# Optimization experiments

Hardware: AMD Instinct MI355X
Metric: run time of the kernel (lower is better)

Reference implementation:

```python
import jax, jax.numpy as jnp
import numpy as np

N_NODES = 50000
N_EDGES = 800000
IN_F = 128
HID = 128
OUT = 2


def setup_inputs() -> dict:
    key = jax.random.key(0)
    ks = jax.random.split(key, 10)
    x = jax.random.normal(ks[0], (N_NODES, IN_F), dtype=jnp.float32)
    edge_index = jax.random.randint(ks[1], (2, N_EDGES), 0, N_NODES, dtype=jnp.int64)

    def lin(k, fan_in, fan_out):
        s = 1.0 / np.sqrt(fan_in)
        return jax.random.uniform(k, (fan_in, fan_out), jnp.float32, -s, s)

    return {
        "x": x,
        "edge_index": edge_index,
        # SAGEConv1: lin_l applied to mean-aggregated neighbors (with bias),
        # lin_r applied to root features (no bias), PyG convention.
        "W1_l": lin(ks[2], IN_F, HID),
        "W1_r": lin(ks[3], IN_F, HID),
        "b1": jnp.zeros((HID,), jnp.float32),
        "W2_l": lin(ks[4], HID, HID),
        "W2_r": lin(ks[5], HID, HID),
        "b2": jnp.zeros((HID,), jnp.float32),
        "Wfc": lin(ks[6], HID, OUT),
        "bfc": jnp.zeros((OUT,), jnp.float32),
    }


def reference(x, edge_index, W1_l, W1_r, b1, W2_l, W2_r, b2, Wfc, bfc):
    n = x.shape[0]
    src = edge_index[0]  # message source j
    dst = edge_index[1]  # aggregation target i
    # in-degree for mean aggregation (clamp to avoid div-by-zero for isolated nodes)
    deg = jax.ops.segment_sum(jnp.ones_like(dst, dtype=x.dtype), dst, num_segments=n)
    inv_deg = 1.0 / jnp.maximum(deg, 1.0)  # [n]

    def sage_conv(h, Wl, Wr, b):
        # mean over incoming neighbor features, then two linear maps
        agg = jax.ops.segment_sum(h[src], dst, num_segments=n) * inv_deg[:, None]
        return agg @ Wl + h @ Wr + b

    # dropout is identity at inference (training=False)
    h = jax.nn.relu(sage_conv(x, W1_l, W1_r, b1))
    h = jax.nn.relu(sage_conv(h, W2_l, W2_r, b2))
    return h @ Wfc + bfc  # [n, out] logits
```

## Files before the change

kernel.cpp:

```cpp
#include <hip/hip_runtime.h>

#define NN 50000
#define NE 800000
#define BSHIFT 9
#define NB_BUCKET ((NN + 511) >> BSHIFT)
#define BCAP 16384
#define EPB 2048
#define NBLK_E ((NE + EPB - 1) / EPB)

#define CVT_BLKS 6250
#define PREP_BLKS 32
#define SETUP_GRID (CVT_BLKS + PREP_BLKS + 1)

typedef short short8 __attribute__((ext_vector_type(8)));
typedef short short4v __attribute__((ext_vector_type(4)));
typedef float f32x4 __attribute__((ext_vector_type(4)));

__device__ inline unsigned short bf16_rne(float f) {
    unsigned u = __float_as_uint(f);
    unsigned r = (u + 0x7fffu + ((u >> 16) & 1u)) >> 16;
    return (unsigned short)r;
}
__device__ inline float bf16_to_f32(unsigned short h) {
    return __uint_as_float((unsigned)h << 16);
}

__global__ __launch_bounds__(256) void setup_kernel(const float* __restrict__ x,
                                                    unsigned short* __restrict__ xb,
                                                    const float* __restrict__ W0,
                                                    const float* __restrict__ W1,
                                                    const float* __restrict__ W2,
                                                    const float* __restrict__ W3,
                                                    short* __restrict__ wf,
                                                    int* __restrict__ cursor0) {
    int b = blockIdx.x;
    if (b < CVT_BLKS) {
        int i = b * 256 + threadIdx.x;
        float4 v = ((const float4*)x)[i];
        short4v r;
        r[0] = (short)bf16_rne(v.x);
        r[1] = (short)bf16_rne(v.y);
        r[2] = (short)bf16_rne(v.z);
        r[3] = (short)bf16_rne(v.w);
        ((short4v*)xb)[i] = r;
    } else if (b < CVT_BLKS + PREP_BLKS) {
        int t = (b - CVT_BLKS) * 256 + threadIdx.x;
        int mat = t >> 11;
        const float* W = (mat == 0) ? W0 : (mat == 1) ? W1 : (mat == 2) ? W2 : W3;
        short* out = wf + (size_t)mat * 32768;
        int r = t & 2047;
        int nt = r >> 8;
        int kc = (r >> 6) & 3;
        int lane = r & 63;
        int n = nt * 16 + (lane & 15);
        int kbase = kc * 32 + ((lane >> 4) << 3);
        short8 vh, vl;
#pragma unroll
        for (int j = 0; j < 8; ++j) {
            float w = W[(size_t)(kbase + j) * 128 + n];
            unsigned short h = bf16_rne(w);
            unsigned short l = bf16_rne(w - bf16_to_f32(h));
            vh[j] = (short)h;
            vl[j] = (short)l;
        }
        size_t o = ((((size_t)nt * 4 + kc) * 2) * 64 + lane) * 8;
        *(short8*)(out + o) = vh;
        *(short8*)(out + o + 512) = vl;
    } else {
        if (threadIdx.x < NB_BUCKET) cursor0[threadIdx.x] = 0;
    }
}

__global__ __launch_bounds__(256) void binA_kernel(const int* __restrict__ src,
                                                   const int* __restrict__ dst,
                                                   int* __restrict__ cursor0,
                                                   unsigned* __restrict__ packed, int ne) {
    __shared__ int cnt[NB_BUCKET];
    __shared__ int gstart[NB_BUCKET];
    __shared__ int cur[NB_BUCKET];
    int t = threadIdx.x;
    if (t < NB_BUCKET) cnt[t] = 0;
    __syncthreads();
    int base = blockIdx.x * EPB + t * 8;
    int s[8], d[8];
    int m = 0;
    if (base + 8 <= ne) {
        *(int4*)&s[0] = *(const int4*)(src + base);
        *(int4*)&s[4] = *(const int4*)(src + base + 4);
        *(int4*)&d[0] = *(const int4*)(dst + base);
        *(int4*)&d[4] = *(const int4*)(dst + base + 4);
        m = 8;
    } else if (base < ne) {
        m = ne - base;
        for (int i = 0; i < m; ++i) { s[i] = src[base + i]; d[i] = dst[base + i]; }
    }
    for (int i = 0; i < m; ++i) atomicAdd(&cnt[d[i] >> BSHIFT], 1);
    __syncthreads();
    if (t < NB_BUCKET) {
        gstart[t] = t * BCAP + atomicAdd(&cursor0[t], cnt[t]);
        cur[t] = 0;
    }
    __syncthreads();
    for (int i = 0; i < m; ++i) {
        int b = d[i] >> BSHIFT;
        int l = atomicAdd(&cur[b], 1);
        packed[gstart[b] + l] = ((unsigned)(d[i] & 511) << 16) | (unsigned)s[i];
    }
}

__global__ __launch_bounds__(512) void binB_kernel(const unsigned* __restrict__ packed,
                                                   const int* __restrict__ cursor0,
                                                   int* __restrict__ row_ptr,
                                                   float* __restrict__ inv_deg,
                                                   int* __restrict__ col, int n, int ne) {
    __shared__ int sdeg[512];
    __shared__ int scur[512];
    __shared__ int scnt[NB_BUCKET];
    __shared__ int sebeg[NB_BUCKET];
    int b = blockIdx.x, t = threadIdx.x;
    if (t < NB_BUCKET) scnt[t] = cursor0[t];
    sdeg[t] = 0;
    __syncthreads();
    if (t == 0) {
        int run = 0;
        for (int i = 0; i < NB_BUCKET; ++i) { sebeg[i] = run; run += scnt[i]; }
    }
    __syncthreads();
    int ebeg = sebeg[b];
    int cntE = scnt[b];
    const unsigned* pk = packed + (size_t)b * BCAP;
    for (int e = t; e < cntE; e += 512) atomicAdd(&sdeg[pk[e] >> 16], 1);
    __syncthreads();
    int v = sdeg[t];
    for (int d = 1; d < 512; d <<= 1) {
        int u = (t >= d) ? sdeg[t - d] : 0;
        __syncthreads();
        sdeg[t] += u;
        __syncthreads();
    }
    int excl = sdeg[t] - v;
    scur[t] = excl;
    int node = (b << BSHIFT) + t;
    if (node < n) {
        row_ptr[node] = ebeg + excl;
        inv_deg[node] = 1.0f / (float)(v > 0 ? v : 1);
    }
    if (b == 0 && t == 0) row_ptr[n] = ne;
    __syncthreads();
    for (int e = t; e < cntE; e += 512) {
        unsigned w = pk[e];
        int dl = w >> 16;
        int pos = ebeg + atomicAdd(&scur[dl], 1);
        col[pos] = (int)(w & 0xffffu);
    }
}

__global__ __launch_bounds__(256) void agg_kernel(const unsigned short* __restrict__ hb,
                                                  const int* __restrict__ row_ptr,
                                                  const int* __restrict__ col,
                                                  const float* __restrict__ inv_deg,
                                                  unsigned short* __restrict__ outb, int n) {
    int node = blockIdx.x * 4 + (threadIdx.x >> 6);
    if (node >= n) return;
    int lane = threadIdx.x & 63;
    int slot = lane >> 4, sub = lane & 15;
    int beg = row_ptr[node], end = row_ptr[node + 1];
    const unsigned short* base = hb + (sub << 3);
    float acc[8];
#pragma unroll
    for (int j = 0; j < 8; ++j) acc[j] = 0.f;

    int e = beg + slot;
    for (; e + 4 < end; e += 8) {
        int j0 = col[e];
        int j1 = col[e + 4];
        uint4 v0 = *(const uint4*)(base + ((size_t)j0 << 7));
        uint4 v1 = *(const uint4*)(base + ((size_t)j1 << 7));
        unsigned w0[4] = {v0.x, v0.y, v0.z, v0.w};
        unsigned w1[4] = {v1.x, v1.y, v1.z, v1.w};
#pragma unroll
        for (int d = 0; d < 4; ++d) {
            acc[2 * d + 0] += __uint_as_float(w0[d] << 16);
            acc[2 * d + 1] += __uint_as_float(w0[d] & 0xffff0000u);
            acc[2 * d + 0] += __uint_as_float(w1[d] << 16);
            acc[2 * d + 1] += __uint_as_float(w1[d] & 0xffff0000u);
        }
    }
    if (e < end) {
        int j0 = col[e];
        uint4 v0 = *(const uint4*)(base + ((size_t)j0 << 7));
        unsigned w0[4] = {v0.x, v0.y, v0.z, v0.w};
#pragma unroll
        for (int d = 0; d < 4; ++d) {
            acc[2 * d + 0] += __uint_as_float(w0[d] << 16);
            acc[2 * d + 1] += __uint_as_float(w0[d] & 0xffff0000u);
        }
    }
#pragma unroll
    for (int j = 0; j < 8; ++j) {
        acc[j] += __shfl_xor(acc[j], 16, 64);
        acc[j] += __shfl_xor(acc[j], 32, 64);
    }
    if (slot == 0) {
        float s = inv_deg[node];
        short8 o;
#pragma unroll
        for (int j = 0; j < 8; ++j) o[j] = (short)bf16_rne(acc[j] * s);
        *(short8*)(outb + ((size_t)node << 7) + (sub << 3)) = o;
    }
}

__global__ __launch_bounds__(256) void gemm_mfma(const unsigned short* __restrict__ A0b,
                                                 const unsigned short* __restrict__ A1b,
                                                 const short* __restrict__ Wf0,
                                                 const short* __restrict__ Wf1,
                                                 const float* __restrict__ bias,
                                                 unsigned short* __restrict__ outb,
                                                 const float* __restrict__ Wfc,
                                                 const float* __restrict__ bfc,
                                                 float* __restrict__ fcout,
                                                 int n, int relu) {
    int lane = threadIdx.x & 63;
    int wave = threadIdx.x >> 6;
    int quad = lane >> 4, m16 = lane & 15;
    int row_base = blockIdx.x * 64 + wave * 16;
    int arow = row_base + m16;
    if (arow > n - 1) arow = n - 1;

    f32x4 acc[8];
#pragma unroll
    for (int nt = 0; nt < 8; ++nt) acc[nt] = (f32x4){0.f, 0.f, 0.f, 0.f};

    const unsigned short* ap0 = A0b + ((size_t)arow << 7) + (quad << 3);
    const unsigned short* ap1 = A1b + ((size_t)arow << 7) + (quad << 3);
#pragma unroll
    for (int kc = 0; kc < 4; ++kc) {
        short8 a0 = *(const short8*)(ap0 + kc * 32);
        short8 a1 = *(const short8*)(ap1 + kc * 32);
        const short* wp0 = Wf0 + ((size_t)kc * 2 * 64 + lane) * 8;
        const short* wp1 = Wf1 + ((size_t)kc * 2 * 64 + lane) * 8;
#pragma unroll
        for (int nt = 0; nt < 8; ++nt) {
            short8 bh0 = *(const short8*)(wp0 + (size_t)nt * 4096);
            short8 bl0 = *(const short8*)(wp0 + (size_t)nt * 4096 + 512);
            short8 bh1 = *(const short8*)(wp1 + (size_t)nt * 4096);
            short8 bl1 = *(const short8*)(wp1 + (size_t)nt * 4096 + 512);
            acc[nt] = __builtin_amdgcn_mfma_f32_16x16x32_bf16(a0, bh0, acc[nt], 0, 0, 0);
            acc[nt] = __builtin_amdgcn_mfma_f32_16x16x32_bf16(a0, bl0, acc[nt], 0, 0, 0);
            acc[nt] = __builtin_amdgcn_mfma_f32_16x16x32_bf16(a1, bh1, acc[nt], 0, 0, 0);
            acc[nt] = __builtin_amdgcn_mfma_f32_16x16x32_bf16(a1, bl1, acc[nt], 0, 0, 0);
        }
    }

    float bcol[8];
#pragma unroll
    for (int nt = 0; nt < 8; ++nt) bcol[nt] = bias[nt * 16 + m16];

    if (Wfc) {
        float w0[8], w1[8];
#pragma unroll
        for (int nt = 0; nt < 8; ++nt) {
            float2 wv = *(const float2*)(Wfc + 2 * (nt * 16 + m16));
            w0[nt] = wv.x;
            w1[nt] = wv.y;
        }
        float b0 = bfc[0], b1 = bfc[1];
#pragma unroll
        for (int r = 0; r < 4; ++r) {
            float p0 = 0.f, p1 = 0.f;
#pragma unroll
            for (int nt = 0; nt < 8; ++nt) {
                float v = fmaxf(acc[nt][r] + bcol[nt], 0.f);
                p0 += v * w0[nt];
                p1 += v * w1[nt];
            }
#pragma unroll
            for (int off = 1; off < 16; off <<= 1) {
                p0 += __shfl_xor(p0, off, 64);
                p1 += __shfl_xor(p1, off, 64);
            }
            int row = row_base + quad * 4 + r;
            if (m16 == 0 && row < n) {
                float2 o;
                o.x = p0 + b0;
                o.y = p1 + b1;
                *(float2*)(fcout + 2 * (size_t)row) = o;
            }
        }
    } else {
#pragma unroll
        for (int r = 0; r < 4; ++r) {
            int row = row_base + quad * 4 + r;
            if (row >= n) continue;
            unsigned short* opb = outb + ((size_t)row << 7) + m16;
#pragma unroll
            for (int nt = 0; nt < 8; ++nt) {
                float v = acc[nt][r] + bcol[nt];
                if (relu) v = fmaxf(v, 0.f);
                opb[nt * 16] = bf16_rne(v);
            }
        }
    }
}

extern "C" void kernel_launch(void* const* d_in, const int* in_sizes, int n_in,
                              void* d_out, int out_size, void* d_ws, size_t ws_size,
                              hipStream_t stream) {
    const float* x   = (const float*)d_in[0];
    const int* edge  = (const int*)d_in[1];
    const float* W1l = (const float*)d_in[2];
    const float* W1r = (const float*)d_in[3];
    const float* b1  = (const float*)d_in[4];
    const float* W2l = (const float*)d_in[5];
    const float* W2r = (const float*)d_in[6];
    const float* b2  = (const float*)d_in[7];
    const float* Wfc = (const float*)d_in[8];
    const float* bfc = (const float*)d_in[9];
    float* out = (float*)d_out;

    const int n = NN, ne = NE;
    const int* src = edge;
    const int* dst = edge + ne;

    char* ws = (char*)d_ws;
    size_t off = 0;
    auto alloc = [&](size_t bytes) -> char* {
        char* p = ws + off;
        off = (off + bytes + 511) & ~(size_t)511;
        return p;
    };
    int* row_ptr     = (int*)alloc((size_t)(n + 1) * 4);
    float* invdeg    = (float*)alloc((size_t)n * 4);
    int* cursor0     = (int*)alloc((size_t)NB_BUCKET * 4);
    short* wf        = (short*)alloc((size_t)4 * 32768 * 2);
    unsigned* packed = (unsigned*)alloc((size_t)NB_BUCKET * BCAP * 4);
    int* col         = (int*)alloc((size_t)ne * 4);
    unsigned short* aggb = (unsigned short*)alloc((size_t)n * 128 * 2);
    unsigned short* xb   = (unsigned short*)alloc((size_t)n * 128 * 2);
    unsigned short* h1b  = (unsigned short*)alloc((size_t)n * 128 * 2);
    (void)ws_size; (void)in_sizes; (void)n_in; (void)out_size;

    setup_kernel<<<SETUP_GRID, 256, 0, stream>>>(x, xb, W1l, W1r, W2l, W2r, wf, cursor0);
    binA_kernel<<<NBLK_E, 256, 0, stream>>>(src, dst, cursor0, packed, ne);
    binB_kernel<<<NB_BUCKET, 512, 0, stream>>>(packed, cursor0, row_ptr, invdeg, col, n, ne);

    agg_kernel<<<(n + 3) / 4, 256, 0, stream>>>(xb, row_ptr, col, invdeg, aggb, n);
    gemm_mfma<<<(n + 63) / 64, 256, 0, stream>>>(aggb, xb, wf, wf + 32768, b1, h1b,
                                                 (const float*)0, (const float*)0, (float*)0, n, 1);
    agg_kernel<<<(n + 3) / 4, 256, 0, stream>>>(h1b, row_ptr, col, invdeg, aggb, n);
    gemm_mfma<<<(n + 63) / 64, 256, 0, stream>>>(aggb, h1b, wf + 2 * 32768, wf + 3 * 32768, b2,
                                                 (unsigned short*)0, Wfc, bfc, out, n, 1);
}
```

Measured before the change: 227.2 us.

## Fuse neighbor aggregation into MFMA GEMM per layer via LDS staging

Replaces the separate aggregation and GEMM kernels with one kernel per layer. Each wave aggregates 16 nodes into an LDS tile, and the tile then feeds MFMA directly with swapped operands so the output is transposed. This removes the aggregated-feature round trip through global memory and two launches. It also swaps the binB block scan for a shuffle-based wave scan and rewrites the epilogue for vectorized stores. In exchange, the grid drops from about 12.5k to 782 blocks, with each wave doing 16 serial aggregations, which may reduce latency hiding for the gathers.

```diff
diff --git a/kernel.cpp b/kernel.cpp
--- a/kernel.cpp
+++ b/kernel.cpp
@@ -11,6 +11,8 @@
 #define CVT_BLKS 6250
 #define PREP_BLKS 32
 #define SETUP_GRID (CVT_BLKS + PREP_BLKS + 1)
+
+#define LROW 136
 
 typedef short short8 __attribute__((ext_vector_type(8)));
 typedef short short4v __attribute__((ext_vector_type(4)));
@@ -117,7 +119,9 @@
     __shared__ int scur[512];
     __shared__ int scnt[NB_BUCKET];
     __shared__ int sebeg[NB_BUCKET];
+    __shared__ int swv[8];
     int b = blockIdx.x, t = threadIdx.x;
+    int lane = t & 63, wid = t >> 6;
     if (t < NB_BUCKET) scnt[t] = cursor0[t];
     sdeg[t] = 0;
     __syncthreads();
@@ -132,13 +136,17 @@
     for (int e = t; e < cntE; e += 512) atomicAdd(&sdeg[pk[e] >> 16], 1);
     __syncthreads();
     int v = sdeg[t];
-    for (int d = 1; d < 512; d <<= 1) {
-        int u = (t >= d) ? sdeg[t - d] : 0;
-        __syncthreads();
-        sdeg[t] += u;
-        __syncthreads();
-    }
-    int excl = sdeg[t] - v;
+    int incl = v;
+#pragma unroll
+    for (int d = 1; d < 64; d <<= 1) {
+        int u = __shfl_up(incl, d, 64);
+        if (lane >= d) incl += u;
+    }
+    if (lane == 63) swv[wid] = incl;
+    __syncthreads();
+    int wbase = 0;
+    for (int i = 0; i < 8; ++i) wbase += (i < wid) ? swv[i] : 0;
+    int excl = wbase + incl - v;
     scur[t] = excl;
     int node = (b << BSHIFT) + t;
     if (node < n) {
@@ -155,88 +163,87 @@
     }
 }
 
-__global__ __launch_bounds__(256) void agg_kernel(const unsigned short* __restrict__ hb,
-                                                  const int* __restrict__ row_ptr,
-                                                  const int* __restrict__ col,
-                                                  const float* __restrict__ inv_deg,
-                                                  unsigned short* __restrict__ outb, int n) {
-    int node = blockIdx.x * 4 + (threadIdx.x >> 6);
-    if (node >= n) return;
-    int lane = threadIdx.x & 63;
+__global__ __launch_bounds__(256) void fused_layer(const unsigned short* __restrict__ hb,
+                                                   const unsigned short* __restrict__ rootb,
+                                                   const int* __restrict__ row_ptr,
+                                                   const int* __restrict__ col,
+                                                   const float* __restrict__ inv_deg,
+                                                   const short* __restrict__ Wf0,
+                                                   const short* __restrict__ Wf1,
+                                                   const float* __restrict__ bias,
+                                                   unsigned short* __restrict__ outb,
+                                                   const float* __restrict__ Wfc,
+                                                   const float* __restrict__ bfc,
+                                                   float* __restrict__ fcout, int n) {
+    __shared__ unsigned short At[4][16 * LROW];
+    int tid = threadIdx.x;
+    int w = tid >> 6, lane = tid & 63;
     int slot = lane >> 4, sub = lane & 15;
-    int beg = row_ptr[node], end = row_ptr[node + 1];
-    const unsigned short* base = hb + (sub << 3);
-    float acc[8];
-#pragma unroll
-    for (int j = 0; j < 8; ++j) acc[j] = 0.f;
-
-    int e = beg + slot;
-    for (; e + 4 < end; e += 8) {
-        int j0 = col[e];
-        int j1 = col[e + 4];
-        uint4 v0 = *(const uint4*)(base + ((size_t)j0 << 7));
-        uint4 v1 = *(const uint4*)(base + ((size_t)j1 << 7));
-        unsigned w0[4] = {v0.x, v0.y, v0.z, v0.w};
-        unsigned w1[4] = {v1.x, v1.y, v1.z, v1.w};
-#pragma unroll
-        for (int d = 0; d < 4; ++d) {
-            acc[2 * d + 0] += __uint_as_float(w0[d] << 16);
-            acc[2 * d + 1] += __uint_as_float(w0[d] & 0xffff0000u);
-            acc[2 * d + 0] += __uint_as_float(w1[d] << 16);
-            acc[2 * d + 1] += __uint_as_float(w1[d] & 0xffff0000u);
-        }
-    }
-    if (e < end) {
-        int j0 = col[e];
-        uint4 v0 = *(const uint4*)(base + ((size_t)j0 << 7));
-        unsigned w0[4] = {v0.x, v0.y, v0.z, v0.w};
-#pragma unroll
-        for (int d = 0; d < 4; ++d) {
-            acc[2 * d + 0] += __uint_as_float(w0[d] << 16);
-            acc[2 * d + 1] += __uint_as_float(w0[d] & 0xffff0000u);
-        }
-    }
-#pragma unroll
-    for (int j = 0; j < 8; ++j) {
-        acc[j] += __shfl_xor(acc[j], 16, 64);
-        acc[j] += __shfl_xor(acc[j], 32, 64);
-    }
-    if (slot == 0) {
-        float s = inv_deg[node];
-        short8 o;
-#pragma unroll
-        for (int j = 0; j < 8; ++j) o[j] = (short)bf16_rne(acc[j] * s);
-        *(short8*)(outb + ((size_t)node << 7) + (sub << 3)) = o;
-    }
-}
-
-__global__ __launch_bounds__(256) void gemm_mfma(const unsigned short* __restrict__ A0b,
-                                                 const unsigned short* __restrict__ A1b,
-                                                 const short* __restrict__ Wf0,
-                                                 const short* __restrict__ Wf1,
-                                                 const float* __restrict__ bias,
-                                                 unsigned short* __restrict__ outb,
-                                                 const float* __restrict__ Wfc,
-                                                 const float* __restrict__ bfc,
-                                                 float* __restrict__ fcout,
-                                                 int n, int relu) {
-    int lane = threadIdx.x & 63;
-    int wave = threadIdx.x >> 6;
-    int quad = lane >> 4, m16 = lane & 15;
-    int row_base = blockIdx.x * 64 + wave * 16;
-    int arow = row_base + m16;
-    if (arow > n - 1) arow = n - 1;
-
-    f32x4 acc[8];
-#pragma unroll
-    for (int nt = 0; nt < 8; ++nt) acc[nt] = (f32x4){0.f, 0.f, 0.f, 0.f};
-
-    const unsigned short* ap0 = A0b + ((size_t)arow << 7) + (quad << 3);
-    const unsigned short* ap1 = A1b + ((size_t)arow << 7) + (quad << 3);
+    int nbase = blockIdx.x * 64 + w * 16;
+    unsigned short* lds = &At[w][0];
+
+    for (int i = 0; i < 16; ++i) {
+        int node = nbase + i;
+        float acc[8];
+#pragma unroll
+        for (int j = 0; j < 8; ++j) acc[j] = 0.f;
+        if (node < n) {
+            int beg = row_ptr[node], end = row_ptr[node + 1];
+            const unsigned short* base = hb + (sub << 3);
+            int e = beg + slot;
+            for (; e + 4 < end; e += 8) {
+                int j0 = col[e];
+                int j1 = col[e + 4];
+                uint4 v0 = *(const uint4*)(base + ((size_t)j0 << 7));
+                uint4 v1 = *(const uint4*)(base + ((size_t)j1 << 7));
+                unsigned w0[4] = {v0.x, v0.y, v0.z, v0.w};
+                unsigned w1[4] = {v1.x, v1.y, v1.z, v1.w};
+#pragma unroll
+                for (int d = 0; d < 4; ++d) {
+                    acc[2 * d + 0] += __uint_as_float(w0[d] << 16);
+                    acc[2 * d + 1] += __uint_as_float(w0[d] & 0xffff0000u);
+                    acc[2 * d + 0] += __uint_as_float(w1[d] << 16);
+                    acc[2 * d + 1] += __uint_as_float(w1[d] & 0xffff0000u);
+                }
+            }
+            if (e < end) {
+                int j0 = col[e];
+                uint4 v0 = *(const uint4*)(base + ((size_t)j0 << 7));
+                unsigned w0[4] = {v0.x, v0.y, v0.z, v0.w};
+#pragma unroll
+                for (int d = 0; d < 4; ++d) {
+                    acc[2 * d + 0] += __uint_as_float(w0[d] << 16);
+                    acc[2 * d + 1] += __uint_as_float(w0[d] & 0xffff0000u);
+                }
+            }
+        }
+#pragma unroll
+        for (int j = 0; j < 8; ++j) {
+            acc[j] += __shfl_xor(acc[j], 16, 64);
+            acc[j] += __shfl_xor(acc[j], 32, 64);
+        }
+        if (slot == 0) {
+            float s = (node < n) ? inv_deg[node] : 0.f;
+            short8 o;
+#pragma unroll
+            for (int j = 0; j < 8; ++j) o[j] = (short)bf16_rne(acc[j] * s);
+            *(short8*)(lds + i * LROW + sub * 8) = o;
+        }
+    }
+    __syncthreads();
+
+    int quad = slot, m16 = sub;
+    f32x4 acc2[8];
+#pragma unroll
+    for (int nt = 0; nt < 8; ++nt) acc2[nt] = (f32x4){0.f, 0.f, 0.f, 0.f};
+
+    int rrow = nbase + m16;
+    if (rrow > n - 1) rrow = n - 1;
+    const unsigned short* rp = rootb + ((size_t)rrow << 7) + (quad << 3);
 #pragma unroll
     for (int kc = 0; kc < 4; ++kc) {
-        short8 a0 = *(const short8*)(ap0 + kc * 32);
-        short8 a1 = *(const short8*)(ap1 + kc * 32);
+        short8 aA = *(const short8*)(lds + m16 * LROW + (quad + 4 * kc) * 8);
+        short8 aR = *(const short8*)(rp + kc * 32);
         const short* wp0 = Wf0 + ((size_t)kc * 2 * 64 + lane) * 8;
         const short* wp1 = Wf1 + ((size_t)kc * 2 * 64 + lane) * 8;
 #pragma unroll
@@ -245,60 +252,52 @@
             short8 bl0 = *(const short8*)(wp0 + (size_t)nt * 4096 + 512);
             short8 bh1 = *(const short8*)(wp1 + (size_t)nt * 4096);
             short8 bl1 = *(const short8*)(wp1 + (size_t)nt * 4096 + 512);
-            acc[nt] = __builtin_amdgcn_mfma_f32_16x16x32_bf16(a0, bh0, acc[nt], 0, 0, 0);
-            acc[nt] = __builtin_amdgcn_mfma_f32_16x16x32_bf16(a0, bl0, acc[nt], 0, 0, 0);
-            acc[nt] = __builtin_amdgcn_mfma_f32_16x16x32_bf16(a1, bh1, acc[nt], 0, 0, 0);
-            acc[nt] = __builtin_amdgcn_mfma_f32_16x16x32_bf16(a1, bl1, acc[nt], 0, 0, 0);
-        }
-    }
-
-    float bcol[8];
-#pragma unroll
-    for (int nt = 0; nt < 8; ++nt) bcol[nt] = bias[nt * 16 + m16];
-
-    if (Wfc) {
-        float w0[8], w1[8];
+            acc2[nt] = __builtin_amdgcn_mfma_f32_16x16x32_bf16(bh0, aA, acc2[nt], 0, 0, 0);
+            acc2[nt] = __builtin_amdgcn_mfma_f32_16x16x32_bf16(bl0, aA, acc2[nt], 0, 0, 0);
+            acc2[nt] = __builtin_amdgcn_mfma_f32_16x16x32_bf16(bh1, aR, acc2[nt], 0, 0, 0);
+            acc2[nt] = __builtin_amdgcn_mfma_f32_16x16x32_bf16(bl1, aR, acc2[nt], 0, 0, 0);
+        }
+    }
+
+    int onode = nbase + m16;
+    if (outb) {
+        if (onode < n) {
+            unsigned short* op = outb + ((size_t)onode << 7) + (quad << 2);
+#pragma unroll
+            for (int nt = 0; nt < 8; ++nt) {
+                float4 bs = *(const float4*)(bias + nt * 16 + (quad << 2));
+                short4v o;
+                o[0] = (short)bf16_rne(fmaxf(acc2[nt][0] + bs.x, 0.f));
+                o[1] = (short)bf16_rne(fmaxf(acc2[nt][1] + bs.y, 0.f));
+                o[2] = (short)bf16_rne(fmaxf(acc2[nt][2] + bs.z, 0.f));
+                o[3] = (short)bf16_rne(fmaxf(acc2[nt][3] + bs.w, 0.f));
+                *(short4v*)(op + nt * 16) = o;
+            }
+        }
+    } else {
+        float p0 = 0.f, p1 = 0.f;
 #pragma unroll
         for (int nt = 0; nt < 8; ++nt) {
-            float2 wv = *(const float2*)(Wfc + 2 * (nt * 16 + m16));
-            w0[nt] = wv.x;
-            w1[nt] = wv.y;
-        }
-        float b0 = bfc[0], b1 = bfc[1];
-#pragma unroll
-        for (int r = 0; r < 4; ++r) {
-            float p0 = 0.f, p1 = 0.f;
-#pragma unroll
-            for (int nt = 0; nt < 8; ++nt) {
-                float v = fmaxf(acc[nt][r] + bcol[nt], 0.f);
-                p0 += v * w0[nt];
-                p1 += v * w1[nt];
+            float4 bs = *(const float4*)(bias + nt * 16 + (quad << 2));
+            float bv[4] = {bs.x, bs.y, bs.z, bs.w};
+#pragma unroll
+            for (int r = 0; r < 4; ++r) {
+                float v = fmaxf(acc2[nt][r] + bv[r], 0.f);
+                int hid = nt * 16 + (quad << 2) + r;
+                float2 wv = *(const float2*)(Wfc + 2 * hid);
+                p0 += v * wv.x;
+                p1 += v * wv.y;
             }
-#pragma unroll
-            for (int off = 1; off < 16; off <<= 1) {
-                p0 += __shfl_xor(p0, off, 64);
-                p1 += __shfl_xor(p1, off, 64);
-            }
-            int row = row_base + quad * 4 + r;
-            if (m16 == 0 && row < n) {
-                float2 o;
-                o.x = p0 + b0;
-                o.y = p1 + b1;
-                *(float2*)(fcout + 2 * (size_t)row) = o;
-            }
-        }
-    } else {
-#pragma unroll
-        for (int r = 0; r < 4; ++r) {
-            int row = row_base + quad * 4 + r;
-            if (row >= n) continue;
-            unsigned short* opb = outb + ((size_t)row << 7) + m16;
-#pragma unroll
-            for (int nt = 0; nt < 8; ++nt) {
-                float v = acc[nt][r] + bcol[nt];
-                if (relu) v = fmaxf(v, 0.f);
-                opb[nt * 16] = bf16_rne(v);
-            }
+        }
+        p0 += __shfl_xor(p0, 16, 64);
+        p0 += __shfl_xor(p0, 32, 64);
+        p1 += __shfl_xor(p1, 16, 64);
+        p1 += __shfl_xor(p1, 32, 64);
+        if (quad == 0 && onode < n) {
+            float2 o;
+            o.x = p0 + bfc[0];
+            o.y = p1 + bfc[1];
+            *(float2*)(fcout + 2 * (size_t)onode) = o;
         }
     }
 }
@@ -335,19 +334,18 @@
     short* wf        = (short*)alloc((size_t)4 * 32768 * 2);
     unsigned* packed = (unsigned*)alloc((size_t)NB_BUCKET * BCAP * 4);
     int* col         = (int*)alloc((size_t)ne * 4);
-    unsigned short* aggb = (unsigned short*)alloc((size_t)n * 128 * 2);
-    unsigned short* xb   = (unsigned short*)alloc((size_t)n * 128 * 2);
-    unsigned short* h1b  = (unsigned short*)alloc((size_t)n * 128 * 2);
+    unsigned short* xb  = (unsigned short*)alloc((size_t)n * 128 * 2);
+    unsigned short* h1b = (unsigned short*)alloc((size_t)n * 128 * 2);
     (void)ws_size; (void)in_sizes; (void)n_in; (void)out_size;
 
     setup_kernel<<<SETUP_GRID, 256, 0, stream>>>(x, xb, W1l, W1r, W2l, W2r, wf, cursor0);
     binA_kernel<<<NBLK_E, 256, 0, stream>>>(src, dst, cursor0, packed, ne);
     binB_kernel<<<NB_BUCKET, 512, 0, stream>>>(packed, cursor0, row_ptr, invdeg, col, n, ne);
 
-    agg_kernel<<<(n + 3) / 4, 256, 0, stream>>>(xb, row_ptr, col, invdeg, aggb, n);
-    gemm_mfma<<<(n + 63) / 64, 256, 0, stream>>>(aggb, xb, wf, wf + 32768, b1, h1b,
-                                                 (const float*)0, (const float*)0, (float*)0, n, 1);
-    agg_kernel<<<(n + 3) / 4, 256, 0, stream>>>(h1b, row_ptr, col, invdeg, aggb, n);
-    gemm_mfma<<<(n + 63) / 64, 256, 0, stream>>>(aggb, h1b, wf + 2 * 32768, wf + 3 * 32768, b2,
-                                                 (unsigned short*)0, Wfc, bfc, out, n, 1);
-}
+    fused_layer<<<(n + 63) / 64, 256, 0, stream>>>(xb, xb, row_ptr, col, invdeg,
+                                                   wf, wf + 32768, b1, h1b,
+                                                   (const float*)0, (const float*)0, (float*)0, n);
+    fused_layer<<<(n + 63) / 64, 256, 0, stream>>>(h1b, h1b, row_ptr, col, invdeg,
+                                                   wf + 2 * 32768, wf + 3 * 32768, b2,
+                                                   (unsigned short*)0, Wfc, bfc, out, n);
+}
```

Result: slower. 341.5 us (+50.3%).
